# Kernel tuning notes

Measured on AMD Instinct MI355X. Metric: run time of the kernel, lower is better.

## Reference

```python
import jax, jax.numpy as jnp
import numpy as np

ROOT_2 = 1.41421
C = 256
DIV = 4
CP = C // DIV  # 64


def _spectral_normalize(w2d):
    # exact largest singular value (torch uses power iteration approx of this)
    s = jnp.linalg.norm(w2d, ord=2)
    return w2d / s


def setup_inputs() -> dict:
    key = jax.random.key(0)
    ks = jax.random.split(key, 10)
    B, H, W = 8, 64, 64
    x = jax.random.normal(ks[0], (B, C, H, W), dtype=jnp.float32)
    # 1x1 conv weights stored as [out, in]; spectral-normalized like torch's spectral_norm
    def conv_w(k, o, i):
        w = jax.random.normal(k, (o, i), dtype=jnp.float32) * (1.0 / np.sqrt(i))
        return _spectral_normalize(w)
    Wq = conv_w(ks[1], CP, C); bq = jnp.zeros((CP,), jnp.float32)
    Wk = conv_w(ks[2], CP, C); bk = jnp.zeros((CP,), jnp.float32)
    Wv = conv_w(ks[3], CP, C); bv = jnp.zeros((CP,), jnp.float32)
    Wo = conv_w(ks[4], C, CP); bo = jnp.zeros((C,), jnp.float32)
    gamma = jnp.zeros((1,), jnp.float32)
    return {"x": x, "Wq": Wq, "bq": bq, "Wk": Wk, "bk": bk,
            "Wv": Wv, "bv": bv, "Wo": Wo, "bo": bo, "gamma": gamma}


def reference(x, Wq, bq, Wk, bk, Wv, bv, Wo, bo, gamma):
    B, c, h, w = x.shape
    n = h * w
    const1 = jnp.float32(ROOT_2 / np.sqrt(C))       # Weight_Scaling(in_channels)
    const2 = jnp.float32(ROOT_2 / np.sqrt(CP))      # Weight_Scaling(in_channels//div_num)
    xs = (const1 * x).reshape(B, c, n)              # [B,C,N]
    q = jnp.einsum('oc,bcn->bon', Wq, xs) + bq[None, :, None]  # [B,C',N]
    k = jnp.einsum('oc,bcn->bon', Wk, xs) + bk[None, :, None]
    v = jnp.einsum('oc,bcn->bon', Wv, xs) + bv[None, :, None]
    # attn[b,i,j] = softmax_j(q[:,i]^T k[:,j])
    scores = jnp.einsum('bcn,bcm->bnm', q, k)       # [B,N,N]
    attn = jax.nn.softmax(scores, axis=-1)
    sa = jnp.einsum('bcm,bnm->bcn', v, attn)        # v @ attn^T
    sa = const2 * sa
    out = jnp.einsum('oc,bcn->bon', Wo, sa) + bo[None, :, None]  # [B,C,N]
    out = out.reshape(B, c, h, w)
    return gamma[0] * out + x
```

## Files before the change

### kernel.cpp

```cpp
#include <hip/hip_runtime.h>


#define Bsz 8
#define Cch 256
#define CPd 64
#define Nn  4096
#define TIL 64

typedef __attribute__((ext_vector_type(8))) short short8;
typedef __attribute__((ext_vector_type(4))) float f32x4;

static constexpr float C1 = (float)(1.41421 / 16.0);
static constexpr float C2 = (float)(1.41421 / 8.0);

__device__ inline unsigned pk_trunc(float lo, float hi) {
    return __builtin_amdgcn_perm(__float_as_uint(hi), __float_as_uint(lo), 0x07060302u);
}

__global__ __launch_bounds__(256) void wconv_kernel(
    const float* __restrict__ Wq, const float* __restrict__ Wk,
    const float* __restrict__ Wv, const float* __restrict__ Wo,
    unsigned short* __restrict__ Wb)
{
    const int idx = (blockIdx.x * 256 + threadIdx.x) * 4;
    const float* src = (idx < 16384) ? Wq : (idx < 32768) ? Wk : (idx < 49152) ? Wv : Wo;
    const float4 v = *(const float4*)(src + (idx & 16383));
    *(uint2*)(Wb + idx) = make_uint2(pk_trunc(v.x, v.y), pk_trunc(v.z, v.w));
}

__global__ __launch_bounds__(256) void qkv_kernel(
    const float* __restrict__ x, const unsigned short* __restrict__ Wb,
    const float* __restrict__ bq, const float* __restrict__ bk, const float* __restrict__ bv,
    unsigned short* __restrict__ qT, unsigned short* __restrict__ kT,
    unsigned short* __restrict__ vB)
{
    __shared__ __align__(16) float T[TIL * 68];

    const int b   = blockIdx.y;
    const int n0  = blockIdx.x * TIL;
    const int t   = threadIdx.x;
    const int g   = t >> 6;
    const int l15 = t & 15;
    const int l4  = (t & 63) >> 4;

    const float* xb = x + (size_t)b * Cch * Nn + n0 + 16 * g + l15;
    short8 xf[8];
    #pragma unroll
    for (int ks = 0; ks < 8; ++ks) {
        float xr[8];
        #pragma unroll
        for (int j = 0; j < 8; ++j)
            xr[j] = C1 * xb[(size_t)(8 * l4 + 32 * ks + j) * Nn];
        union { unsigned u[4]; short8 s; } p;
        p.u[0] = pk_trunc(xr[0], xr[1]); p.u[1] = pk_trunc(xr[2], xr[3]);
        p.u[2] = pk_trunc(xr[4], xr[5]); p.u[3] = pk_trunc(xr[6], xr[7]);
        xf[ks] = p.s;
    }

    #pragma unroll
    for (int mat = 0; mat < 3; ++mat) {
        const unsigned short* W = Wb + mat * 16384;
        const float* bias = (mat == 0) ? bq : (mat == 1) ? bk : bv;

        f32x4 acc[4];
        #pragma unroll
        for (int st = 0; st < 4; ++st) {
            const float bb = bias[16 * st + l15];
            acc[st] = (f32x4){bb, bb, bb, bb};
        }
        #pragma unroll
        for (int st = 0; st < 4; ++st) {
            #pragma unroll
            for (int ks = 0; ks < 8; ++ks) {
                const short8 wf = *(const short8*)&W[(16 * st + l15) * Cch + 8 * l4 + 32 * ks];
                acc[st] = __builtin_amdgcn_mfma_f32_16x16x32_bf16(xf[ks], wf, acc[st], 0, 0, 0);
            }
        }

        __syncthreads();
        if (mat < 2) {
            #pragma unroll
            for (int st = 0; st < 4; ++st)
                #pragma unroll
                for (int r = 0; r < 4; ++r)
                    T[(16 * g + 4 * l4 + r) * 68 + 16 * st + l15] = acc[st][r];
        } else {
            #pragma unroll
            for (int st = 0; st < 4; ++st)
                #pragma unroll
                for (int r = 0; r < 4; ++r)
                    T[(16 * st + l15) * 68 + 16 * g + 4 * l4 + r] = acc[st][r];
        }
        __syncthreads();

        const int row = t >> 2;
        const int sg  = 16 * (t & 3);
        const float4 a0 = *(const float4*)&T[row * 68 + sg + 0];
        const float4 a1 = *(const float4*)&T[row * 68 + sg + 4];
        const float4 a2 = *(const float4*)&T[row * 68 + sg + 8];
        const float4 a3 = *(const float4*)&T[row * 68 + sg + 12];
        const uint4 lo = make_uint4(pk_trunc(a0.x, a0.y), pk_trunc(a0.z, a0.w),
                                    pk_trunc(a1.x, a1.y), pk_trunc(a1.z, a1.w));
        const uint4 hi = make_uint4(pk_trunc(a2.x, a2.y), pk_trunc(a2.z, a2.w),
                                    pk_trunc(a3.x, a3.y), pk_trunc(a3.z, a3.w));
        unsigned short* dst;
        if (mat < 2) {
            dst = (mat == 0 ? qT : kT) + ((size_t)(b * Nn + n0 + row)) * CPd + sg;
        } else {
            dst = vB + ((size_t)(b * CPd + row)) * Nn + n0 + sg;
        }
        *(uint4*)dst = lo;
        *(uint4*)(dst + 8) = hi;
    }
}

__global__ __launch_bounds__(256) void flash_kernel(
    const unsigned short* __restrict__ qT, const unsigned short* __restrict__ kT,
    const unsigned short* __restrict__ vB, float* __restrict__ sa_t)
{
    __shared__ __align__(16) unsigned short Qs[TIL * 72];
    __shared__ __align__(16) unsigned short Ks[TIL * 72];
    __shared__ __align__(16) unsigned short Vs[TIL * 72];
    __shared__ __align__(16) float Ps[TIL * 68];
    __shared__ float Lsh[TIL];

    const int b   = blockIdx.y;
    const int n0  = blockIdx.x * TIL;
    const int t   = threadIdx.x;
    const int l   = t & 63;
    const int g   = t >> 6;
    const int l15 = l & 15;
    const int l4  = l >> 4;

    {
        const uint4* qg = (const uint4*)(qT + (size_t)(b * Nn + n0) * CPd);
        int r = t >> 3, cc = t & 7;
        uint4 v0 = qg[r * 8 + cc];
        uint4 v1 = qg[(r + 32) * 8 + cc];
        *(uint4*)&Qs[r * 72 + 8 * cc]        = v0;
        *(uint4*)&Qs[(r + 32) * 72 + 8 * cc] = v1;
    }
    if (t < TIL) Lsh[t] = 0.f;
    __syncthreads();

    const short8 qf0 = *(const short8*)&Qs[(16 * g + l15) * 72 + 8 * l4];
    const short8 qf1 = *(const short8*)&Qs[(16 * g + l15) * 72 + 8 * l4 + 32];

    f32x4 acco[4];
    #pragma unroll
    for (int ct = 0; ct < 4; ++ct) acco[ct] = (f32x4){0.f, 0.f, 0.f, 0.f};
    float Lp[4] = {0.f, 0.f, 0.f, 0.f};

    const uint4* kg = (const uint4*)(kT + (size_t)b * Nn * CPd);
    const unsigned short* vb = vB + (size_t)b * CPd * Nn;

    for (int m0 = 0; m0 < Nn; m0 += TIL) {
        __syncthreads();
        {
            int r = t >> 3, cc = t & 7;
            uint4 k0 = kg[(m0 + r) * 8 + cc];
            uint4 k1 = kg[(m0 + r + 32) * 8 + cc];
            *(uint4*)&Ks[r * 72 + 8 * cc]        = k0;
            *(uint4*)&Ks[(r + 32) * 72 + 8 * cc] = k1;
            uint4 w0 = *(const uint4*)(vb + (size_t)r * Nn + m0 + 8 * cc);
            uint4 w1 = *(const uint4*)(vb + (size_t)(r + 32) * Nn + m0 + 8 * cc);
            *(uint4*)&Vs[r * 72 + 8 * cc]        = w0;
            *(uint4*)&Vs[(r + 32) * 72 + 8 * cc] = w1;
        }
        __syncthreads();

        f32x4 accs[4];
        #pragma unroll
        for (int st = 0; st < 4; ++st) {
            accs[st] = (f32x4){0.f, 0.f, 0.f, 0.f};
            const short8 kf0 = *(const short8*)&Ks[(16 * st + l15) * 72 + 8 * l4];
            const short8 kf1 = *(const short8*)&Ks[(16 * st + l15) * 72 + 8 * l4 + 32];
            accs[st] = __builtin_amdgcn_mfma_f32_16x16x32_bf16(qf0, kf0, accs[st], 0, 0, 0);
            accs[st] = __builtin_amdgcn_mfma_f32_16x16x32_bf16(qf1, kf1, accs[st], 0, 0, 0);
        }

        #pragma unroll
        for (int st = 0; st < 4; ++st) {
            #pragma unroll
            for (int r = 0; r < 4; ++r) {
                float p = __expf(accs[st][r]);
                Lp[r] += p;
                Ps[(16 * g + 4 * l4 + r) * 68 + 16 * st + l15] = p;
            }
        }
        __syncthreads();

        #pragma unroll
        for (int ks = 0; ks < 2; ++ks) {
            const float4 a0 = *(const float4*)&Ps[(16 * g + l15) * 68 + 8 * l4 + 32 * ks];
            const float4 a1 = *(const float4*)&Ps[(16 * g + l15) * 68 + 8 * l4 + 32 * ks + 4];
            union { unsigned u[4]; short8 s; } pu;
            pu.u[0] = pk_trunc(a0.x, a0.y); pu.u[1] = pk_trunc(a0.z, a0.w);
            pu.u[2] = pk_trunc(a1.x, a1.y); pu.u[3] = pk_trunc(a1.z, a1.w);
            #pragma unroll
            for (int ct = 0; ct < 4; ++ct) {
                const short8 vf = *(const short8*)&Vs[(16 * ct + l15) * 72 + 8 * l4 + 32 * ks];
                acco[ct] = __builtin_amdgcn_mfma_f32_16x16x32_bf16(pu.s, vf, acco[ct], 0, 0, 0);
            }
        }
    }

    #pragma unroll
    for (int r = 0; r < 4; ++r) atomicAdd(&Lsh[16 * g + 4 * l4 + r], Lp[r]);
    __syncthreads();

    float* sab = sa_t + (size_t)(b * Nn + n0) * CPd;
    #pragma unroll
    for (int r = 0; r < 4; ++r) {
        const float sc = C2 / Lsh[16 * g + 4 * l4 + r];
        #pragma unroll
        for (int ct = 0; ct < 4; ++ct)
            sab[(size_t)(16 * g + 4 * l4 + r) * CPd + 16 * ct + l15] = acco[ct][r] * sc;
    }
}

__global__ __launch_bounds__(256) void out_kernel(
    const float* __restrict__ sa_t, const unsigned short* __restrict__ Wob,
    const float* __restrict__ bo, const float* __restrict__ gamma,
    const float* __restrict__ x, float* __restrict__ y)
{
    __shared__ __align__(16) unsigned short Wos[Cch * 72];
    __shared__ __align__(16) unsigned short Sas[TIL * 72];
    __shared__ float bos[Cch];

    const int b   = blockIdx.y;
    const int n0  = blockIdx.x * TIL;
    const int t   = threadIdx.x;
    const int l   = t & 63;
    const int g   = t >> 6;
    const int l15 = l & 15;
    const int l4  = l >> 4;

    bos[t] = bo[t];
    {
        const uint4* wg = (const uint4*)Wob;
        #pragma unroll
        for (int p = 0; p < 8; ++p) {
            const int idx = p * 256 + t;
            const int row = idx >> 3, seg = idx & 7;
            *(uint4*)&Wos[row * 72 + seg * 8] = wg[idx];
        }
        const float* sab = sa_t + (size_t)(b * Nn + n0) * CPd;
        const int n = t >> 2, seg = t & 3;
        const float4* sr = (const float4*)(sab + (size_t)n * CPd + seg * 16);
        float4 s0 = sr[0], s1 = sr[1], s2 = sr[2], s3 = sr[3];
        *(uint4*)&Sas[n * 72 + seg * 16] =
            make_uint4(pk_trunc(s0.x, s0.y), pk_trunc(s0.z, s0.w),
                       pk_trunc(s1.x, s1.y), pk_trunc(s1.z, s1.w));
        *(uint4*)&Sas[n * 72 + seg * 16 + 8] =
            make_uint4(pk_trunc(s2.x, s2.y), pk_trunc(s2.z, s2.w),
                       pk_trunc(s3.x, s3.y), pk_trunc(s3.z, s3.w));
    }
    __syncthreads();

    short8 bfr[4][2];
    #pragma unroll
    for (int ns = 0; ns < 4; ++ns) {
        bfr[ns][0] = *(const short8*)&Sas[(16 * ns + l15) * 72 + 8 * l4];
        bfr[ns][1] = *(const short8*)&Sas[(16 * ns + l15) * 72 + 8 * l4 + 32];
    }
    const float gam = gamma[0];
    const float* xb = x + (size_t)b * Cch * Nn;
    float*       yb = y + (size_t)b * Cch * Nn;

    #pragma unroll
    for (int os = 0; os < 4; ++os) {
        const int obase = 64 * g + 16 * os;
        const short8 af0 = *(const short8*)&Wos[(obase + l15) * 72 + 8 * l4];
        const short8 af1 = *(const short8*)&Wos[(obase + l15) * 72 + 8 * l4 + 32];
        #pragma unroll
        for (int ns = 0; ns < 4; ++ns) {
            f32x4 acc = (f32x4){0.f, 0.f, 0.f, 0.f};
            acc = __builtin_amdgcn_mfma_f32_16x16x32_bf16(af0, bfr[ns][0], acc, 0, 0, 0);
            acc = __builtin_amdgcn_mfma_f32_16x16x32_bf16(af1, bfr[ns][1], acc, 0, 0, 0);
            #pragma unroll
            for (int r = 0; r < 4; ++r) {
                const int o = obase + 4 * l4 + r;
                const size_t idx = (size_t)o * Nn + n0 + 16 * ns + l15;
                yb[idx] = fmaf(gam, acc[r] + bos[o], xb[idx]);
            }
        }
    }
}

extern "C" void kernel_launch(void* const* d_in, const int* in_sizes, int n_in,
                              void* d_out, int out_size, void* d_ws, size_t ws_size,
                              hipStream_t stream)
{
    (void)in_sizes; (void)n_in; (void)out_size; (void)ws_size;
    const float* x     = (const float*)d_in[0];
    const float* Wq    = (const float*)d_in[1];
    const float* bq    = (const float*)d_in[2];
    const float* Wk    = (const float*)d_in[3];
    const float* bk    = (const float*)d_in[4];
    const float* Wv    = (const float*)d_in[5];
    const float* bv    = (const float*)d_in[6];
    const float* Wo    = (const float*)d_in[7];
    const float* bo    = (const float*)d_in[8];
    const float* gamma = (const float*)d_in[9];
    float* y = (float*)d_out;

    const size_t per = (size_t)Bsz * Nn * CPd;
    unsigned short* qT = (unsigned short*)d_ws;
    unsigned short* kT = qT + per;
    unsigned short* vB = kT + per;
    float* sa = (float*)(vB + per);
    unsigned short* Wb = (unsigned short*)(sa + per);

    dim3 grid(Nn / TIL, Bsz);
    wconv_kernel<<<64, 256, 0, stream>>>(Wq, Wk, Wv, Wo, Wb);
    qkv_kernel<<<grid, 256, 0, stream>>>(x, Wb, bq, bk, bv, qT, kT, vB);
    flash_kernel<<<grid, 256, 0, stream>>>(qT, kT, vB, sa);
    out_kernel<<<grid, 256, 0, stream>>>(sa, Wb + 3 * 16384, bo, gamma, x, y);
}
```

Before: 223.0 us.

## Switch flash attention kernel to 32x32x16 MFMA with bf16-packed P tile

Restructures the attention kernel so each wave computes a 32x32 tile using 32x32x16 bf16 MFMA instructions instead of 16x16x32. Q fragments are kept in registers loaded straight from global memory, which removes the Q shared-memory staging. Probabilities are packed to bf16 in registers using a DPP lane swap and byte permute, then written to a smaller shared buffer. This halves LDS traffic for P and drops the float P tile. It adds launch bounds for 4 blocks per CU, at the cost of more accumulator registers per thread.

Result: slower. 270.9 us (+21.5%).

```diff
diff --git a/kernel.cpp b/kernel.cpp
--- a/kernel.cpp
+++ b/kernel.cpp
@@ -7,14 +7,19 @@
 #define Nn  4096
 #define TIL 64
 
-typedef __attribute__((ext_vector_type(8))) short short8;
-typedef __attribute__((ext_vector_type(4))) float f32x4;
+typedef __attribute__((ext_vector_type(8)))  short short8;
+typedef __attribute__((ext_vector_type(4)))  float f32x4;
+typedef __attribute__((ext_vector_type(16))) float f32x16;
 
 static constexpr float C1 = (float)(1.41421 / 16.0);
 static constexpr float C2 = (float)(1.41421 / 8.0);
 
 __device__ inline unsigned pk_trunc(float lo, float hi) {
     return __builtin_amdgcn_perm(__float_as_uint(hi), __float_as_uint(lo), 0x07060302u);
+}
+__device__ inline float dpp_swap1(float v) {
+    return __uint_as_float((unsigned)__builtin_amdgcn_mov_dpp(
+        (int)__float_as_uint(v), 0xB1, 0xF, 0xF, true));
 }
 
 __global__ __launch_bounds__(256) void wconv_kernel(
@@ -114,50 +119,49 @@
     }
 }
 
-__global__ __launch_bounds__(256) void flash_kernel(
+__global__ __launch_bounds__(256, 4) void flash_kernel(
     const unsigned short* __restrict__ qT, const unsigned short* __restrict__ kT,
     const unsigned short* __restrict__ vB, float* __restrict__ sa_t)
 {
-    __shared__ __align__(16) unsigned short Qs[TIL * 72];
     __shared__ __align__(16) unsigned short Ks[TIL * 72];
     __shared__ __align__(16) unsigned short Vs[TIL * 72];
-    __shared__ __align__(16) float Ps[TIL * 68];
+    __shared__ __align__(16) unsigned Pb[TIL * 40];
     __shared__ float Lsh[TIL];
 
     const int b   = blockIdx.y;
     const int n0  = blockIdx.x * TIL;
     const int t   = threadIdx.x;
     const int l   = t & 63;
-    const int g   = t >> 6;
-    const int l15 = l & 15;
-    const int l4  = l >> 4;
-
+    const int w   = t >> 6;
+    const int nh  = w & 1;
+    const int mq  = w >> 1;
+    const int l31 = l & 31;
+    const int l1  = l >> 5;
+
+    if (t < TIL) Lsh[t] = 0.f;
+
+    short8 qf[4];
     {
-        const uint4* qg = (const uint4*)(qT + (size_t)(b * Nn + n0) * CPd);
-        int r = t >> 3, cc = t & 7;
-        uint4 v0 = qg[r * 8 + cc];
-        uint4 v1 = qg[(r + 32) * 8 + cc];
-        *(uint4*)&Qs[r * 72 + 8 * cc]        = v0;
-        *(uint4*)&Qs[(r + 32) * 72 + 8 * cc] = v1;
-    }
-    if (t < TIL) Lsh[t] = 0.f;
-    __syncthreads();
-
-    const short8 qf0 = *(const short8*)&Qs[(16 * g + l15) * 72 + 8 * l4];
-    const short8 qf1 = *(const short8*)&Qs[(16 * g + l15) * 72 + 8 * l4 + 32];
-
-    f32x4 acco[4];
-    #pragma unroll
-    for (int ct = 0; ct < 4; ++ct) acco[ct] = (f32x4){0.f, 0.f, 0.f, 0.f};
-    float Lp[4] = {0.f, 0.f, 0.f, 0.f};
+        const unsigned short* qp = qT + (size_t)(b * Nn + n0 + 32 * nh + l31) * CPd + 8 * l1;
+        #pragma unroll
+        for (int kc = 0; kc < 4; ++kc) qf[kc] = *(const short8*)(qp + 16 * kc);
+    }
+
+    f32x16 acco;
+    float Lp[16];
+    #pragma unroll
+    for (int r = 0; r < 16; ++r) { acco[r] = 0.f; Lp[r] = 0.f; }
 
     const uint4* kg = (const uint4*)(kT + (size_t)b * Nn * CPd);
     const unsigned short* vb = vB + (size_t)b * CPd * Nn;
+    const unsigned sel = (l & 1) ? 0x03020706u : 0x07060302u;
+    const int par  = l & 1;
+    const int colp = 16 * mq + (l31 >> 1);
 
     for (int m0 = 0; m0 < Nn; m0 += TIL) {
         __syncthreads();
         {
-            int r = t >> 3, cc = t & 7;
+            const int r = t >> 3, cc = t & 7;
             uint4 k0 = kg[(m0 + r) * 8 + cc];
             uint4 k1 = kg[(m0 + r + 32) * 8 + cc];
             *(uint4*)&Ks[r * 72 + 8 * cc]        = k0;
@@ -169,53 +173,51 @@
         }
         __syncthreads();
 
-        f32x4 accs[4];
-        #pragma unroll
-        for (int st = 0; st < 4; ++st) {
-            accs[st] = (f32x4){0.f, 0.f, 0.f, 0.f};
-            const short8 kf0 = *(const short8*)&Ks[(16 * st + l15) * 72 + 8 * l4];
-            const short8 kf1 = *(const short8*)&Ks[(16 * st + l15) * 72 + 8 * l4 + 32];
-            accs[st] = __builtin_amdgcn_mfma_f32_16x16x32_bf16(qf0, kf0, accs[st], 0, 0, 0);
-            accs[st] = __builtin_amdgcn_mfma_f32_16x16x32_bf16(qf1, kf1, accs[st], 0, 0, 0);
-        }
-
-        #pragma unroll
-        for (int st = 0; st < 4; ++st) {
-            #pragma unroll
-            for (int r = 0; r < 4; ++r) {
-                float p = __expf(accs[st][r]);
-                Lp[r] += p;
-                Ps[(16 * g + 4 * l4 + r) * 68 + 16 * st + l15] = p;
+        f32x16 accs;
+        #pragma unroll
+        for (int r = 0; r < 16; ++r) accs[r] = 0.f;
+        #pragma unroll
+        for (int kc = 0; kc < 4; ++kc) {
+            const short8 kf = *(const short8*)&Ks[(32 * mq + l31) * 72 + 16 * kc + 8 * l1];
+            accs = __builtin_amdgcn_mfma_f32_32x32x16_bf16(qf[kc], kf, accs, 0, 0, 0);
+        }
+
+        unsigned u[16];
+        #pragma unroll
+        for (int r = 0; r < 16; ++r) {
+            float p = __expf(accs[r]);
+            Lp[r] += p;
+            float nb = dpp_swap1(p);
+            u[r] = __builtin_amdgcn_perm(__float_as_uint(nb), __float_as_uint(p), sel);
+        }
+        {
+            const int rb = 32 * nh + 4 * l1 + 2 * par;
+            #pragma unroll
+            for (int q = 0; q < 4; ++q) {
+                Pb[(rb + 8 * q) * 40 + colp]     = u[4 * q + 2 * par];
+                Pb[(rb + 8 * q + 1) * 40 + colp] = u[4 * q + 2 * par + 1];
             }
         }
         __syncthreads();
 
         #pragma unroll
-        for (int ks = 0; ks < 2; ++ks) {
-            const float4 a0 = *(const float4*)&Ps[(16 * g + l15) * 68 + 8 * l4 + 32 * ks];
-            const float4 a1 = *(const float4*)&Ps[(16 * g + l15) * 68 + 8 * l4 + 32 * ks + 4];
-            union { unsigned u[4]; short8 s; } pu;
-            pu.u[0] = pk_trunc(a0.x, a0.y); pu.u[1] = pk_trunc(a0.z, a0.w);
-            pu.u[2] = pk_trunc(a1.x, a1.y); pu.u[3] = pk_trunc(a1.z, a1.w);
-            #pragma unroll
-            for (int ct = 0; ct < 4; ++ct) {
-                const short8 vf = *(const short8*)&Vs[(16 * ct + l15) * 72 + 8 * l4 + 32 * ks];
-                acco[ct] = __builtin_amdgcn_mfma_f32_16x16x32_bf16(pu.s, vf, acco[ct], 0, 0, 0);
-            }
-        }
-    }
-
-    #pragma unroll
-    for (int r = 0; r < 4; ++r) atomicAdd(&Lsh[16 * g + 4 * l4 + r], Lp[r]);
+        for (int ks = 0; ks < 4; ++ks) {
+            const short8 pf = *(const short8*)&Pb[(32 * nh + l31) * 40 + 8 * ks + 4 * l1];
+            const short8 vf = *(const short8*)&Vs[(32 * mq + l31) * 72 + 16 * ks + 8 * l1];
+            acco = __builtin_amdgcn_mfma_f32_32x32x16_bf16(pf, vf, acco, 0, 0, 0);
+        }
+    }
+
+    #pragma unroll
+    for (int r = 0; r < 16; ++r)
+        atomicAdd(&Lsh[32 * nh + (r & 3) + 8 * (r >> 2) + 4 * l1], Lp[r]);
     __syncthreads();
 
     float* sab = sa_t + (size_t)(b * Nn + n0) * CPd;
     #pragma unroll
-    for (int r = 0; r < 4; ++r) {
-        const float sc = C2 / Lsh[16 * g + 4 * l4 + r];
-        #pragma unroll
-        for (int ct = 0; ct < 4; ++ct)
-            sab[(size_t)(16 * g + 4 * l4 + r) * CPd + 16 * ct + l15] = acco[ct][r] * sc;
+    for (int r = 0; r < 16; ++r) {
+        const int nl = 32 * nh + (r & 3) + 8 * (r >> 2) + 4 * l1;
+        sab[(size_t)nl * CPd + 32 * mq + l31] = acco[r] * (C2 / Lsh[nl]);
     }
 }
 
```

## Split flash attention over key range and combine partial sums in out kernel

Applied to the files above, without the earlier changes.

Splits the key dimension of the attention kernel into two halves across a third grid dimension. This doubles the block count from 512 to 1024 so the GPU's compute units are better occupied. Each split writes unnormalized partial outputs and row sums, and the output kernel sums both partials and normalizes before the projection. Q fragments are now loaded straight from global memory instead of through shared memory, and launch bounds request 4 blocks per SM. The cost is extra workspace and more global traffic for the partial outputs. The combine relies on the softmax having no max subtraction, which the code already assumed.

Result: faster. 211.6 us (-5.1%).

```diff
diff --git a/kernel.cpp b/kernel.cpp
--- a/kernel.cpp
+++ b/kernel.cpp
@@ -6,6 +6,8 @@
 #define CPd 64
 #define Nn  4096
 #define TIL 64
+#define NSPL 2
+#define MHALF (Nn / NSPL)
 
 typedef __attribute__((ext_vector_type(8))) short short8;
 typedef __attribute__((ext_vector_type(4))) float f32x4;
@@ -114,11 +116,10 @@
     }
 }
 
-__global__ __launch_bounds__(256) void flash_kernel(
+__global__ __launch_bounds__(256, 4) void flash_kernel(
     const unsigned short* __restrict__ qT, const unsigned short* __restrict__ kT,
-    const unsigned short* __restrict__ vB, float* __restrict__ sa_t)
-{
-    __shared__ __align__(16) unsigned short Qs[TIL * 72];
+    const unsigned short* __restrict__ vB, float* __restrict__ Op, float* __restrict__ Lg)
+{
     __shared__ __align__(16) unsigned short Ks[TIL * 72];
     __shared__ __align__(16) unsigned short Vs[TIL * 72];
     __shared__ __align__(16) float Ps[TIL * 68];
@@ -126,25 +127,18 @@
 
     const int b   = blockIdx.y;
     const int n0  = blockIdx.x * TIL;
+    const int s   = blockIdx.z;
     const int t   = threadIdx.x;
     const int l   = t & 63;
     const int g   = t >> 6;
     const int l15 = l & 15;
     const int l4  = l >> 4;
 
-    {
-        const uint4* qg = (const uint4*)(qT + (size_t)(b * Nn + n0) * CPd);
-        int r = t >> 3, cc = t & 7;
-        uint4 v0 = qg[r * 8 + cc];
-        uint4 v1 = qg[(r + 32) * 8 + cc];
-        *(uint4*)&Qs[r * 72 + 8 * cc]        = v0;
-        *(uint4*)&Qs[(r + 32) * 72 + 8 * cc] = v1;
-    }
     if (t < TIL) Lsh[t] = 0.f;
-    __syncthreads();
-
-    const short8 qf0 = *(const short8*)&Qs[(16 * g + l15) * 72 + 8 * l4];
-    const short8 qf1 = *(const short8*)&Qs[(16 * g + l15) * 72 + 8 * l4 + 32];
+
+    const unsigned short* qp = qT + (size_t)(b * Nn + n0 + 16 * g + l15) * CPd + 8 * l4;
+    const short8 qf0 = *(const short8*)qp;
+    const short8 qf1 = *(const short8*)(qp + 32);
 
     f32x4 acco[4];
     #pragma unroll
@@ -153,11 +147,13 @@
 
     const uint4* kg = (const uint4*)(kT + (size_t)b * Nn * CPd);
     const unsigned short* vb = vB + (size_t)b * CPd * Nn;
-
-    for (int m0 = 0; m0 < Nn; m0 += TIL) {
+    const int mbase = s * MHALF;
+
+    for (int mi = 0; mi < MHALF; mi += TIL) {
+        const int m0 = mbase + mi;
         __syncthreads();
         {
-            int r = t >> 3, cc = t & 7;
+            const int r = t >> 3, cc = t & 7;
             uint4 k0 = kg[(m0 + r) * 8 + cc];
             uint4 k1 = kg[(m0 + r + 32) * 8 + cc];
             *(uint4*)&Ks[r * 72 + 8 * cc]        = k0;
@@ -194,13 +190,13 @@
         for (int ks = 0; ks < 2; ++ks) {
             const float4 a0 = *(const float4*)&Ps[(16 * g + l15) * 68 + 8 * l4 + 32 * ks];
             const float4 a1 = *(const float4*)&Ps[(16 * g + l15) * 68 + 8 * l4 + 32 * ks + 4];
-            union { unsigned u[4]; short8 s; } pu;
+            union { unsigned u[4]; short8 s8; } pu;
             pu.u[0] = pk_trunc(a0.x, a0.y); pu.u[1] = pk_trunc(a0.z, a0.w);
             pu.u[2] = pk_trunc(a1.x, a1.y); pu.u[3] = pk_trunc(a1.z, a1.w);
             #pragma unroll
             for (int ct = 0; ct < 4; ++ct) {
                 const short8 vf = *(const short8*)&Vs[(16 * ct + l15) * 72 + 8 * l4 + 32 * ks];
-                acco[ct] = __builtin_amdgcn_mfma_f32_16x16x32_bf16(pu.s, vf, acco[ct], 0, 0, 0);
+                acco[ct] = __builtin_amdgcn_mfma_f32_16x16x32_bf16(pu.s8, vf, acco[ct], 0, 0, 0);
             }
         }
     }
@@ -209,18 +205,20 @@
     for (int r = 0; r < 4; ++r) atomicAdd(&Lsh[16 * g + 4 * l4 + r], Lp[r]);
     __syncthreads();
 
-    float* sab = sa_t + (size_t)(b * Nn + n0) * CPd;
+    float* ob = Op + ((size_t)(s * Bsz + b) * Nn + n0) * CPd;
     #pragma unroll
     for (int r = 0; r < 4; ++r) {
-        const float sc = C2 / Lsh[16 * g + 4 * l4 + r];
+        const int nl = 16 * g + 4 * l4 + r;
         #pragma unroll
         for (int ct = 0; ct < 4; ++ct)
-            sab[(size_t)(16 * g + 4 * l4 + r) * CPd + 16 * ct + l15] = acco[ct][r] * sc;
-    }
+            ob[(size_t)nl * CPd + 16 * ct + l15] = acco[ct][r];
+    }
+    if (t < TIL) Lg[(size_t)(s * Bsz + b) * Nn + n0 + t] = Lsh[t];
 }
 
 __global__ __launch_bounds__(256) void out_kernel(
-    const float* __restrict__ sa_t, const unsigned short* __restrict__ Wob,
+    const float* __restrict__ Op, const float* __restrict__ Lg,
+    const unsigned short* __restrict__ Wob,
     const float* __restrict__ bo, const float* __restrict__ gamma,
     const float* __restrict__ x, float* __restrict__ y)
 {
@@ -245,16 +243,22 @@
             const int row = idx >> 3, seg = idx & 7;
             *(uint4*)&Wos[row * 72 + seg * 8] = wg[idx];
         }
-        const float* sab = sa_t + (size_t)(b * Nn + n0) * CPd;
         const int n = t >> 2, seg = t & 3;
-        const float4* sr = (const float4*)(sab + (size_t)n * CPd + seg * 16);
-        float4 s0 = sr[0], s1 = sr[1], s2 = sr[2], s3 = sr[3];
-        *(uint4*)&Sas[n * 72 + seg * 16] =
-            make_uint4(pk_trunc(s0.x, s0.y), pk_trunc(s0.z, s0.w),
-                       pk_trunc(s1.x, s1.y), pk_trunc(s1.z, s1.w));
-        *(uint4*)&Sas[n * 72 + seg * 16 + 8] =
-            make_uint4(pk_trunc(s2.x, s2.y), pk_trunc(s2.z, s2.w),
-                       pk_trunc(s3.x, s3.y), pk_trunc(s3.z, s3.w));
+        const float* o0 = Op + ((size_t)(b * Nn + n0 + n)) * CPd + seg * 16;
+        const float* o1 = o0 + (size_t)Bsz * Nn * CPd;
+        const float l0 = Lg[(size_t)b * Nn + n0 + n];
+        const float l1 = Lg[(size_t)(Bsz + b) * Nn + n0 + n];
+        const float sc = C2 / (l0 + l1);
+        unsigned pk[8];
+        #pragma unroll
+        for (int i = 0; i < 4; ++i) {
+            const float4 a = ((const float4*)o0)[i];
+            const float4 c = ((const float4*)o1)[i];
+            pk[2 * i]     = pk_trunc((a.x + c.x) * sc, (a.y + c.y) * sc);
+            pk[2 * i + 1] = pk_trunc((a.z + c.z) * sc, (a.w + c.w) * sc);
+        }
+        *(uint4*)&Sas[n * 72 + seg * 16]     = make_uint4(pk[0], pk[1], pk[2], pk[3]);
+        *(uint4*)&Sas[n * 72 + seg * 16 + 8] = make_uint4(pk[4], pk[5], pk[6], pk[7]);
     }
     __syncthreads();
 
@@ -309,12 +313,14 @@
     unsigned short* qT = (unsigned short*)d_ws;
     unsigned short* kT = qT + per;
     unsigned short* vB = kT + per;
-    float* sa = (float*)(vB + per);
-    unsigned short* Wb = (unsigned short*)(sa + per);
+    float* Op = (float*)(vB + per);
+    float* Lg = Op + NSPL * per;
+    unsigned short* Wb = (unsigned short*)(Lg + NSPL * Bsz * Nn);
 
     dim3 grid(Nn / TIL, Bsz);
+    dim3 gridF(Nn / TIL, Bsz, NSPL);
     wconv_kernel<<<64, 256, 0, stream>>>(Wq, Wk, Wv, Wo, Wb);
     qkv_kernel<<<grid, 256, 0, stream>>>(x, Wb, bq, bk, bv, qT, kT, vB);
-    flash_kernel<<<grid, 256, 0, stream>>>(qT, kT, vB, sa);
-    out_kernel<<<grid, 256, 0, stream>>>(sa, Wb + 3 * 16384, bo, gamma, x, y);
-}
+    flash_kernel<<<gridF, 256, 0, stream>>>(qT, kT, vB, Op, Lg);
+    out_kernel<<<grid, 256, 0, stream>>>(Op, Lg, Wb + 3 * 16384, bo, gamma, x, y);
+}
```
